# Optimization experiments

Hardware: AMD Instinct MI355X
Metric: run time of the kernel (lower is better)

The kernel has to match this reference:

```python
import jax, jax.numpy as jnp
import numpy as np

N = 4096      # batch size (PK-sampled)
D = 1024      # feature dim
K = 4         # instances per identity
NUM_IDS = N // K


def setup_inputs() -> dict:
    key = jax.random.key(0)
    inputs = jax.random.normal(key, (N, D), dtype=jnp.float32)
    # PK-structured labels: NUM_IDS identities, K instances each.
    targets = jnp.repeat(jnp.arange(NUM_IDS, dtype=jnp.int32), K)
    # Flags alternate within each identity -> every (same/diff id) x (same/diff flag)
    # combination is non-empty for every anchor row.
    flags = jnp.tile(jnp.array([0, 1, 0, 1], dtype=jnp.int32), N // 4)
    epoch = 10  # unused by the loss, kept for signature fidelity
    return {"inputs": inputs, "targets": targets, "flags": flags, "epoch": epoch}


def reference(inputs, targets, flags, epoch):
    # Pairwise Euclidean distances: ||a||^2 + ||b||^2 - 2 a.b, clamped + sqrt.
    sq = jnp.sum(inputs * inputs, axis=1, keepdims=True)          # [n,1]
    dist = sq + sq.T - 2.0 * (inputs @ inputs.T)                   # [n,n]
    dist = jnp.sqrt(jnp.clip(dist, 1e-12, None))

    same_id = targets[:, None] == targets[None, :]                 # mask_1
    same_fl = flags[:, None] == flags[None, :]                     # mask_2
    m_same_hp = same_id & same_fl
    m_same_hn = (~same_id) & same_fl
    m_dif_hp = same_id & (~same_fl)
    m_dif_hn = (~same_id) & (~same_fl)

    NEG = jnp.asarray(-jnp.inf, dist.dtype)
    POS = jnp.asarray(jnp.inf, dist.dtype)
    dist_same_ap = jnp.max(jnp.where(m_same_hp, dist, NEG), axis=1)
    dist_same_an = jnp.min(jnp.where(m_same_hn, dist, POS), axis=1)
    dist_dif_ap = jnp.max(jnp.where(m_dif_hp, dist, NEG), axis=1)
    dist_dif_an = jnp.min(jnp.where(m_dif_hn, dist, POS), axis=1)

    # torch: first index in the FULL row equal to the masked min (exact equality)
    same_min_idx = jnp.argmax(dist == dist_same_an[:, None], axis=1)  # [n]
    dif_min_idx = jnp.argmax(dist == dist_dif_an[:, None], axis=1)    # [n]
    dist_dif_neg = dist[same_min_idx, dif_min_idx]                    # [n]

    relu = jax.nn.relu
    # MarginRankingLoss(x1, x2, y=1) = mean(relu(x2 - x1 + margin))
    loss_same = jnp.mean(relu(dist_same_ap - dist_same_an + 0.8))
    loss_dif = jnp.mean(relu(dist_dif_ap - dist_dif_an + 0.5))
    loss_neg = jnp.mean(relu(dist_same_ap - dist_dif_neg + 0.3))
    return loss_same + loss_dif + loss_neg
```

## Files before the change

### kernel.cpp

```cpp
#include <hip/hip_runtime.h>

#define NROWS 4096
#define DIM   1024

using f32x4 = __attribute__((ext_vector_type(4))) float;
using bfrag = __attribute__((ext_vector_type(8))) short;

__device__ __forceinline__ unsigned short f2bf(float f) {
  unsigned u = __float_as_uint(f);
  u += 0x7fffu + ((u >> 16) & 1u);
  return (unsigned short)(u >> 16);
}
__device__ __forceinline__ float bf2f(unsigned short b) {
  return __uint_as_float(((unsigned)b) << 16);
}
__device__ __forceinline__ unsigned long long shflx64(unsigned long long v, int m) {
  int lo = __shfl_xor((int)(unsigned)(v & 0xffffffffull), m);
  int hi = __shfl_xor((int)(unsigned)(v >> 32), m);
  return ((unsigned long long)(unsigned)hi << 32) | (unsigned)lo;
}

__global__ void prep_kernel(const float* __restrict__ X, unsigned short* __restrict__ Xb,
                            float* __restrict__ sqv, int* maxS, int* maxD,
                            unsigned long long* minS, unsigned long long* minD,
                            float* out) {
  int row = blockIdx.x, t = threadIdx.x;
  float4 v = reinterpret_cast<const float4*>(X + (size_t)row * DIM)[t];
  unsigned short b0 = f2bf(v.x), b1 = f2bf(v.y), b2 = f2bf(v.z), b3 = f2bf(v.w);
  float f0 = bf2f(b0), f1 = bf2f(b1), f2 = bf2f(b2), f3 = bf2f(b3);
  float s = f0 * f0 + f1 * f1 + f2 * f2 + f3 * f3;
  reinterpret_cast<ushort4*>(Xb + (size_t)row * DIM)[t] = make_ushort4(b0, b1, b2, b3);
  for (int m = 32; m; m >>= 1) s += __shfl_xor(s, m);
  __shared__ float ws4[4];
  if ((t & 63) == 0) ws4[t >> 6] = s;
  __syncthreads();
  if (t == 0) {
    sqv[row] = (ws4[0] + ws4[1]) + (ws4[2] + ws4[3]);
    maxS[row] = 0; maxD[row] = 0; minS[row] = ~0ull; minD[row] = ~0ull;
    if (row == 0) out[0] = 0.f;
  }
}

__global__ __launch_bounds__(256, 4) void gram_kernel(
    const unsigned short* __restrict__ Xb, const float* __restrict__ sqv,
    const int* __restrict__ tg, const int* __restrict__ fl,
    int* maxS, int* maxD, unsigned long long* minS, unsigned long long* minD) {
  __shared__ __attribute__((aligned(16))) char smem[32768];
  __shared__ float srow[128], scol[128];
  __shared__ int rtagp[128], ctagp[128];

  int tm = 0, g = blockIdx.x, rem = 32;
  while (g >= rem) { g -= rem; rem--; tm++; }
  int tn = tm + g;
  const int row0 = tm * 128, col0 = tn * 128;
  const int tid = threadIdx.x;
  const int wave = tid >> 6, lane = tid & 63;
  const int q = lane >> 4, li = lane & 15;

  if (tid < 128) {
    srow[tid] = sqv[row0 + tid];
    rtagp[tid] = (fl[row0 + tid] << 12) | tg[row0 + tid];
  } else {
    int c = tid - 128;
    scol[c] = sqv[col0 + c];
    ctagp[c] = (fl[col0 + c] << 12) | tg[col0 + c];
  }

  unsigned short (*As)[64] = (unsigned short (*)[64])smem;
  unsigned short (*Bs)[64] = (unsigned short (*)[64])(smem + 16384);
  float* Ds = (float*)smem;

  f32x4 acc[4][4] = {};
  const int wr = (wave >> 1) * 64, wc = (wave & 1) * 64;
  const int ksrc = ((lane & 7) ^ (lane >> 3)) * 8;

  for (int ks = 0; ks < DIM; ks += 64) {
    __syncthreads();
#pragma unroll
    for (int qq = 0; qq < 4; ++qq) {
      int base = (wave * 4 + qq) * 1024;
      int r = (base >> 7) + (lane >> 3);
      const unsigned short* srcA = Xb + (size_t)(row0 + r) * DIM + ks + ksrc;
      __builtin_amdgcn_global_load_lds(
          (const __attribute__((address_space(1))) void*)srcA,
          (__attribute__((address_space(3))) void*)(smem + base), 16, 0, 0);
      const unsigned short* srcB = Xb + (size_t)(col0 + r) * DIM + ks + ksrc;
      __builtin_amdgcn_global_load_lds(
          (const __attribute__((address_space(1))) void*)srcB,
          (__attribute__((address_space(3))) void*)(smem + 16384 + base), 16, 0, 0);
    }
    __syncthreads();
#pragma unroll
    for (int kk = 0; kk < 2; ++kk) {
      bfrag a[4], b[4];
      int kel = ((kk * 4 + q) ^ (lane & 7)) * 8;
#pragma unroll
      for (int m = 0; m < 4; ++m)
        a[m] = *(const bfrag*)&As[wr + m * 16 + li][kel];
#pragma unroll
      for (int n = 0; n < 4; ++n)
        b[n] = *(const bfrag*)&Bs[wc + n * 16 + li][kel];
#pragma unroll
      for (int m = 0; m < 4; ++m)
#pragma unroll
        for (int n = 0; n < 4; ++n)
          acc[m][n] = __builtin_amdgcn_mfma_f32_16x16x32_bf16(a[m], b[n], acc[m][n], 0, 0, 0);
    }
  }
  __syncthreads();

  float cmxS[4], cmxD[4];
  unsigned long long cmnS[4], cmnD[4];
#pragma unroll
  for (int n = 0; n < 4; ++n) { cmxS[n] = -1.f; cmxD[n] = -1.f; cmnS[n] = ~0ull; cmnD[n] = ~0ull; }
  int ctv[4]; float scv[4];
#pragma unroll
  for (int n = 0; n < 4; ++n) { int lc = wc + n * 16 + li; ctv[n] = ctagp[lc]; scv[n] = scol[lc]; }

#pragma unroll
  for (int h = 0; h < 2; ++h) {
    if ((wave >> 1) == h) {
#pragma unroll
      for (int m = 0; m < 4; ++m)
#pragma unroll
        for (int r = 0; r < 4; ++r) {
          int lr = wr + m * 16 + q * 4 + r;
          int rl = lr & 63;
          int rt = rtagp[lr];
          float sr = srow[lr];
          unsigned long long rbase = (unsigned)(row0 + lr);
#pragma unroll
          for (int n = 0; n < 4; ++n) {
            float d = sqrtf(fmaxf(sr + scv[n] - 2.0f * acc[m][n][r], 1e-12f));
            Ds[rl * 128 + ((wc + n * 16 + li) ^ (lr & 31))] = d;
            int x = rt ^ ctv[n];
            unsigned long long pk = ((unsigned long long)__float_as_uint(d) << 32) | rbase;
            if ((x & 0xFFF) == 0) {
              if ((x >> 12) == 0) cmxS[n] = fmaxf(cmxS[n], d);
              else                cmxD[n] = fmaxf(cmxD[n], d);
            } else {
              if ((x >> 12) == 0) { if (pk < cmnS[n]) cmnS[n] = pk; }
              else                { if (pk < cmnD[n]) cmnD[n] = pk; }
            }
          }
        }
    }
    __syncthreads();
    {
      int rl = (wave & 1) * 32 + (lane & 31);
      int j = (wave >> 1) * 2 + (lane >> 5);
      int rt = rtagp[h * 64 + rl];
      float mxS = -1.f, mxD = -1.f;
      unsigned long long mnS = ~0ull, mnD = ~0ull;
      for (int i = 0; i < 32; ++i) {
        int c = j * 32 + i;
        float d = Ds[rl * 128 + (c ^ (rl & 31))];
        int x = rt ^ ctagp[c];
        unsigned long long pk =
            ((unsigned long long)__float_as_uint(d) << 32) | (unsigned)(col0 + c);
        if ((x & 0xFFF) == 0) { if ((x >> 12) == 0) mxS = fmaxf(mxS, d); else mxD = fmaxf(mxD, d); }
        else { if ((x >> 12) == 0) { if (pk < mnS) mnS = pk; } else { if (pk < mnD) mnD = pk; } }
      }
      mxS = fmaxf(mxS, __shfl_xor(mxS, 32));
      mxD = fmaxf(mxD, __shfl_xor(mxD, 32));
      unsigned long long o = shflx64(mnS, 32); if (o < mnS) mnS = o;
      o = shflx64(mnD, 32); if (o < mnD) mnD = o;
      if (lane < 32) {
        int gr = row0 + h * 64 + rl;
        atomicMax(&maxS[gr], __float_as_int(mxS));
        atomicMax(&maxD[gr], __float_as_int(mxD));
        atomicMin(&minS[gr], mnS);
        atomicMin(&minD[gr], mnD);
      }
    }
    __syncthreads();
  }

#pragma unroll
  for (int n = 0; n < 4; ++n) {
    cmxS[n] = fmaxf(cmxS[n], __shfl_xor(cmxS[n], 16));
    cmxD[n] = fmaxf(cmxD[n], __shfl_xor(cmxD[n], 16));
    unsigned long long o = shflx64(cmnS[n], 16); if (o < cmnS[n]) cmnS[n] = o;
    o = shflx64(cmnD[n], 16); if (o < cmnD[n]) cmnD[n] = o;
    cmxS[n] = fmaxf(cmxS[n], __shfl_xor(cmxS[n], 32));
    cmxD[n] = fmaxf(cmxD[n], __shfl_xor(cmxD[n], 32));
    o = shflx64(cmnS[n], 32); if (o < cmnS[n]) cmnS[n] = o;
    o = shflx64(cmnD[n], 32); if (o < cmnD[n]) cmnD[n] = o;
    if (lane < 16) {
      int gc = col0 + wc + n * 16 + lane;
      atomicMax(&maxS[gc], __float_as_int(cmxS[n]));
      atomicMax(&maxD[gc], __float_as_int(cmxD[n]));
      atomicMin(&minS[gc], cmnS[n]);
      atomicMin(&minD[gc], cmnD[n]);
    }
  }
}

__global__ void finish_kernel(const unsigned short* __restrict__ Xb,
                              const float* __restrict__ sqv,
                              const int* __restrict__ maxS, const int* __restrict__ maxD,
                              const unsigned long long* __restrict__ minS,
                              const unsigned long long* __restrict__ minD, float* out) {
  int wave = threadIdx.x >> 6, lane = threadIdx.x & 63;
  float part = 0.f;
  for (int rr = 0; rr < 8; ++rr) {
    int row = blockIdx.x * 32 + wave * 8 + rr;
    unsigned long long pS = minS[row], pD = minD[row];
    int ia = (int)(pS & 0xffffffffull);
    int ib = (int)(pD & 0xffffffffull);
    const ushort4* pa = (const ushort4*)(Xb + (size_t)ia * DIM);
    const ushort4* pb = (const ushort4*)(Xb + (size_t)ib * DIM);
    float s = 0.f;
#pragma unroll
    for (int qq = 0; qq < 4; ++qq) {
      ushort4 a = pa[lane + qq * 64], b = pb[lane + qq * 64];
      s += bf2f(a.x) * bf2f(b.x) + bf2f(a.y) * bf2f(b.y) +
           bf2f(a.z) * bf2f(b.z) + bf2f(a.w) * bf2f(b.w);
    }
    for (int m = 32; m; m >>= 1) s += __shfl_xor(s, m);
    if (lane == 0) {
      float dneg = sqrtf(fmaxf(sqv[ia] + sqv[ib] - 2.f * s, 1e-12f));
      float mS = __int_as_float(maxS[row]);
      float mD = __int_as_float(maxD[row]);
      float mnSv = __uint_as_float((unsigned)(pS >> 32));
      float mnDv = __uint_as_float((unsigned)(pD >> 32));
      part += fmaxf(mS - mnSv + 0.8f, 0.f) + fmaxf(mD - mnDv + 0.5f, 0.f) +
              fmaxf(mS - dneg + 0.3f, 0.f);
    }
  }
  __shared__ float wp[4];
  if (lane == 0) wp[wave] = part;
  __syncthreads();
  if (threadIdx.x == 0)
    atomicAdd(out, ((wp[0] + wp[1]) + (wp[2] + wp[3])) * (1.0f / 4096.0f));
}

extern "C" void kernel_launch(void* const* d_in, const int* in_sizes, int n_in,
                              void* d_out, int out_size, void* d_ws, size_t ws_size,
                              hipStream_t stream) {
  const float* X = (const float*)d_in[0];
  const int* tg  = (const int*)d_in[1];
  const int* fl  = (const int*)d_in[2];
  float* out = (float*)d_out;

  char* w = (char*)d_ws;
  unsigned short* Xb = (unsigned short*)(w);
  float* sqv = (float*)(w + 8388608);
  int* maxS  = (int*)(w + 8404992);
  int* maxD  = (int*)(w + 8421376);
  unsigned long long* minS = (unsigned long long*)(w + 8437760);
  unsigned long long* minD = (unsigned long long*)(w + 8470528);

  prep_kernel<<<NROWS, 256, 0, stream>>>(X, Xb, sqv, maxS, maxD, minS, minD, out);
  gram_kernel<<<528, 256, 0, stream>>>(Xb, sqv, tg, fl, maxS, maxD, minS, minD);
  finish_kernel<<<128, 256, 0, stream>>>(Xb, sqv, maxS, maxD, minS, minD, out);
}
```

Baseline: 165.9 us.

## Double-buffer gram K-loop, remap tile order, and move column reduction into half-loop

Replaces the single-buffered 64-wide K loop with a double-buffered 32-wide pipeline. The next stage's global-to-LDS load is issued before the MFMA body on the current buffer, so each step needs one barrier instead of two. The LDS layout changes to a k-chunk-major arrangement without the XOR swizzle, and triangular tile indices are computed by sqrt with an interleaved block ordering. Per-column reduction state now lives only inside the active half, to cut register pressure, and launch bounds drop to 3 waves per SIMD. Risks include LDS bank conflicts from the unswizzled layout and lower occupancy.

```diff
diff --git a/kernel.cpp b/kernel.cpp
--- a/kernel.cpp
+++ b/kernel.cpp
@@ -41,7 +41,36 @@
   }
 }
 
-__global__ __launch_bounds__(256, 4) void gram_kernel(
+#define STAGE(BASE, KS)                                                         \
+  {                                                                             \
+    _Pragma("unroll")                                                           \
+    for (int qp = 0; qp < 2; ++qp) {                                            \
+      int ldso = (wave * 2 + qp) * 1024;                                        \
+      int rsrc = qp * 64 + lane;                                                \
+      const unsigned short* sA = Xb + (size_t)(row0 + rsrc) * DIM + (KS) + wave * 8; \
+      __builtin_amdgcn_global_load_lds(                                         \
+          (const __attribute__((address_space(1))) void*)sA,                    \
+          (__attribute__((address_space(3))) void*)((BASE) + ldso), 16, 0, 0);  \
+      const unsigned short* sB = Xb + (size_t)(col0 + rsrc) * DIM + (KS) + wave * 8; \
+      __builtin_amdgcn_global_load_lds(                                         \
+          (const __attribute__((address_space(1))) void*)sB,                    \
+          (__attribute__((address_space(3))) void*)((BASE) + 8192 + ldso), 16, 0, 0); \
+    }                                                                           \
+  }
+
+#define BODY(BASE)                                                              \
+  {                                                                             \
+    bfrag a[4], b[4];                                                           \
+    _Pragma("unroll") for (int m = 0; m < 4; ++m)                               \
+      a[m] = *(const bfrag*)((BASE) + q * 2048 + (wr + m * 16 + li) * 16);      \
+    _Pragma("unroll") for (int n = 0; n < 4; ++n)                               \
+      b[n] = *(const bfrag*)((BASE) + 8192 + q * 2048 + (wc + n * 16 + li) * 16); \
+    _Pragma("unroll") for (int m = 0; m < 4; ++m)                               \
+      _Pragma("unroll") for (int n = 0; n < 4; ++n)                             \
+        acc[m][n] = __builtin_amdgcn_mfma_f32_16x16x32_bf16(a[m], b[n], acc[m][n], 0, 0, 0); \
+  }
+
+__global__ __launch_bounds__(256, 3) void gram_kernel(
     const unsigned short* __restrict__ Xb, const float* __restrict__ sqv,
     const int* __restrict__ tg, const int* __restrict__ fl,
     int* maxS, int* maxD, unsigned long long* minS, unsigned long long* minD) {
@@ -49,9 +78,11 @@
   __shared__ float srow[128], scol[128];
   __shared__ int rtagp[128], ctagp[128];
 
-  int tm = 0, g = blockIdx.x, rem = 32;
-  while (g >= rem) { g -= rem; rem--; tm++; }
-  int tn = tm + g;
+  int g = (blockIdx.x & 7) * 66 + (blockIdx.x >> 3);
+  int tn = (int)((sqrtf(8.f * g + 1.f) - 1.f) * 0.5f);
+  while ((tn + 1) * (tn + 2) / 2 <= g) ++tn;
+  while (tn * (tn + 1) / 2 > g) --tn;
+  int tm = g - tn * (tn + 1) / 2;
   const int row0 = tm * 128, col0 = tn * 128;
   const int tid = threadIdx.x;
   const int wave = tid >> 6, lane = tid & 63;
@@ -66,60 +97,36 @@
     ctagp[c] = (fl[col0 + c] << 12) | tg[col0 + c];
   }
 
-  unsigned short (*As)[64] = (unsigned short (*)[64])smem;
-  unsigned short (*Bs)[64] = (unsigned short (*)[64])(smem + 16384);
+  char* B0 = smem;
+  char* B1 = smem + 16384;
   float* Ds = (float*)smem;
 
   f32x4 acc[4][4] = {};
   const int wr = (wave >> 1) * 64, wc = (wave & 1) * 64;
-  const int ksrc = ((lane & 7) ^ (lane >> 3)) * 8;
-
-  for (int ks = 0; ks < DIM; ks += 64) {
-    __syncthreads();
-#pragma unroll
-    for (int qq = 0; qq < 4; ++qq) {
-      int base = (wave * 4 + qq) * 1024;
-      int r = (base >> 7) + (lane >> 3);
-      const unsigned short* srcA = Xb + (size_t)(row0 + r) * DIM + ks + ksrc;
-      __builtin_amdgcn_global_load_lds(
-          (const __attribute__((address_space(1))) void*)srcA,
-          (__attribute__((address_space(3))) void*)(smem + base), 16, 0, 0);
-      const unsigned short* srcB = Xb + (size_t)(col0 + r) * DIM + ks + ksrc;
-      __builtin_amdgcn_global_load_lds(
-          (const __attribute__((address_space(1))) void*)srcB,
-          (__attribute__((address_space(3))) void*)(smem + 16384 + base), 16, 0, 0);
-    }
-    __syncthreads();
-#pragma unroll
-    for (int kk = 0; kk < 2; ++kk) {
-      bfrag a[4], b[4];
-      int kel = ((kk * 4 + q) ^ (lane & 7)) * 8;
-#pragma unroll
-      for (int m = 0; m < 4; ++m)
-        a[m] = *(const bfrag*)&As[wr + m * 16 + li][kel];
-#pragma unroll
-      for (int n = 0; n < 4; ++n)
-        b[n] = *(const bfrag*)&Bs[wc + n * 16 + li][kel];
-#pragma unroll
-      for (int m = 0; m < 4; ++m)
-#pragma unroll
-        for (int n = 0; n < 4; ++n)
-          acc[m][n] = __builtin_amdgcn_mfma_f32_16x16x32_bf16(a[m], b[n], acc[m][n], 0, 0, 0);
-    }
-  }
+
+  STAGE(B0, 0);
   __syncthreads();
-
-  float cmxS[4], cmxD[4];
-  unsigned long long cmnS[4], cmnD[4];
-#pragma unroll
-  for (int n = 0; n < 4; ++n) { cmxS[n] = -1.f; cmxD[n] = -1.f; cmnS[n] = ~0ull; cmnD[n] = ~0ull; }
-  int ctv[4]; float scv[4];
-#pragma unroll
-  for (int n = 0; n < 4; ++n) { int lc = wc + n * 16 + li; ctv[n] = ctagp[lc]; scv[n] = scol[lc]; }
+  for (int tt = 0; tt < 16; ++tt) {
+    int s0 = tt * 2;
+    STAGE(B1, (s0 + 1) * 32);
+    BODY(B0);
+    __syncthreads();
+    if (tt < 15) STAGE(B0, (s0 + 2) * 32);
+    BODY(B1);
+    __syncthreads();
+  }
 
 #pragma unroll
   for (int h = 0; h < 2; ++h) {
     if ((wave >> 1) == h) {
+      float cmxS[4], cmxD[4];
+      unsigned long long cmnS[4], cmnD[4];
+      int ctv[4]; float scv[4];
+#pragma unroll
+      for (int n = 0; n < 4; ++n) {
+        cmxS[n] = -1.f; cmxD[n] = -1.f; cmnS[n] = ~0ull; cmnD[n] = ~0ull;
+        int lc = wc + n * 16 + li; ctv[n] = ctagp[lc]; scv[n] = scol[lc];
+      }
 #pragma unroll
       for (int m = 0; m < 4; ++m)
 #pragma unroll
@@ -132,7 +139,7 @@
 #pragma unroll
           for (int n = 0; n < 4; ++n) {
             float d = sqrtf(fmaxf(sr + scv[n] - 2.0f * acc[m][n][r], 1e-12f));
-            Ds[rl * 128 + ((wc + n * 16 + li) ^ (lr & 31))] = d;
+            Ds[rl * 128 + ((wc + n * 16 + li) ^ (rl & 31))] = d;
             int x = rt ^ ctv[n];
             unsigned long long pk = ((unsigned long long)__float_as_uint(d) << 32) | rbase;
             if ((x & 0xFFF) == 0) {
@@ -144,6 +151,24 @@
             }
           }
         }
+#pragma unroll
+      for (int n = 0; n < 4; ++n) {
+        cmxS[n] = fmaxf(cmxS[n], __shfl_xor(cmxS[n], 16));
+        cmxD[n] = fmaxf(cmxD[n], __shfl_xor(cmxD[n], 16));
+        unsigned long long o = shflx64(cmnS[n], 16); if (o < cmnS[n]) cmnS[n] = o;
+        o = shflx64(cmnD[n], 16); if (o < cmnD[n]) cmnD[n] = o;
+        cmxS[n] = fmaxf(cmxS[n], __shfl_xor(cmxS[n], 32));
+        cmxD[n] = fmaxf(cmxD[n], __shfl_xor(cmxD[n], 32));
+        o = shflx64(cmnS[n], 32); if (o < cmnS[n]) cmnS[n] = o;
+        o = shflx64(cmnD[n], 32); if (o < cmnD[n]) cmnD[n] = o;
+        if (lane < 16) {
+          int gc = col0 + wc + n * 16 + lane;
+          atomicMax(&maxS[gc], __float_as_int(cmxS[n]));
+          atomicMax(&maxD[gc], __float_as_int(cmxD[n]));
+          atomicMin(&minS[gc], cmnS[n]);
+          atomicMin(&minD[gc], cmnD[n]);
+        }
+      }
     }
     __syncthreads();
     {
@@ -174,25 +199,6 @@
       }
     }
     __syncthreads();
-  }
-
-#pragma unroll
-  for (int n = 0; n < 4; ++n) {
-    cmxS[n] = fmaxf(cmxS[n], __shfl_xor(cmxS[n], 16));
-    cmxD[n] = fmaxf(cmxD[n], __shfl_xor(cmxD[n], 16));
-    unsigned long long o = shflx64(cmnS[n], 16); if (o < cmnS[n]) cmnS[n] = o;
-    o = shflx64(cmnD[n], 16); if (o < cmnD[n]) cmnD[n] = o;
-    cmxS[n] = fmaxf(cmxS[n], __shfl_xor(cmxS[n], 32));
-    cmxD[n] = fmaxf(cmxD[n], __shfl_xor(cmxD[n], 32));
-    o = shflx64(cmnS[n], 32); if (o < cmnS[n]) cmnS[n] = o;
-    o = shflx64(cmnD[n], 32); if (o < cmnD[n]) cmnD[n] = o;
-    if (lane < 16) {
-      int gc = col0 + wc + n * 16 + lane;
-      atomicMax(&maxS[gc], __float_as_int(cmxS[n]));
-      atomicMax(&maxD[gc], __float_as_int(cmxD[n]));
-      atomicMin(&minS[gc], cmnS[n]);
-      atomicMin(&minD[gc], cmnD[n]);
-    }
   }
 }
 
```

New measurement: 188.4 us. 13.6% more time.

## Replace LDS-staged row reduction in gram epilogue with register shuffles

Applied to the files above, without the earlier changes.

The epilogue no longer writes the distance tile to shared memory and re-reads it for the per-row max/min. Each lane now keeps per-row partial reductions in registers, combines them across the 16 column lanes with xor shuffles, and issues row atomics from lane li==0. This drops the two-phase LDS pass and its barriers, at the cost of more shuffles and more row atomics (one per wave per row instead of one per row per half-tile). The launch-bounds occupancy hint of 4 is also removed, and the staging loop is moved into a macro.

```diff
diff --git a/kernel.cpp b/kernel.cpp
--- a/kernel.cpp
+++ b/kernel.cpp
@@ -41,7 +41,24 @@
   }
 }
 
-__global__ __launch_bounds__(256, 4) void gram_kernel(
+#define STAGE(KS)                                                                \
+  {                                                                              \
+    _Pragma("unroll")                                                            \
+    for (int qq = 0; qq < 4; ++qq) {                                             \
+      int boff = (wave * 4 + qq) * 1024;                     \
+      int r = (wave * 4 + qq) * 8 + (lane >> 3);        \
+      const unsigned short* sA = Xb + (size_t)(row0 + r) * DIM + (KS) + ksrc;    \
+      __builtin_amdgcn_global_load_lds(                                          \
+          (const __attribute__((address_space(1))) void*)sA,                     \
+          (__attribute__((address_space(3))) void*)(smem + boff), 16, 0, 0);     \
+      const unsigned short* sB = Xb + (size_t)(col0 + r) * DIM + (KS) + ksrc;    \
+      __builtin_amdgcn_global_load_lds(                                          \
+          (const __attribute__((address_space(1))) void*)sB,                     \
+          (__attribute__((address_space(3))) void*)(smem + 16384 + boff), 16, 0, 0); \
+    }                                                                            \
+  }
+
+__global__ __launch_bounds__(256) void gram_kernel(
     const unsigned short* __restrict__ Xb, const float* __restrict__ sqv,
     const int* __restrict__ tg, const int* __restrict__ fl,
     int* maxS, int* maxD, unsigned long long* minS, unsigned long long* minD) {
@@ -56,6 +73,7 @@
   const int tid = threadIdx.x;
   const int wave = tid >> 6, lane = tid & 63;
   const int q = lane >> 4, li = lane & 15;
+  const int ksrc = ((lane & 7) ^ (lane >> 3)) * 8;
 
   if (tid < 128) {
     srow[tid] = sqv[row0 + tid];
@@ -68,27 +86,13 @@
 
   unsigned short (*As)[64] = (unsigned short (*)[64])smem;
   unsigned short (*Bs)[64] = (unsigned short (*)[64])(smem + 16384);
-  float* Ds = (float*)smem;
 
   f32x4 acc[4][4] = {};
   const int wr = (wave >> 1) * 64, wc = (wave & 1) * 64;
-  const int ksrc = ((lane & 7) ^ (lane >> 3)) * 8;
 
   for (int ks = 0; ks < DIM; ks += 64) {
     __syncthreads();
-#pragma unroll
-    for (int qq = 0; qq < 4; ++qq) {
-      int base = (wave * 4 + qq) * 1024;
-      int r = (base >> 7) + (lane >> 3);
-      const unsigned short* srcA = Xb + (size_t)(row0 + r) * DIM + ks + ksrc;
-      __builtin_amdgcn_global_load_lds(
-          (const __attribute__((address_space(1))) void*)srcA,
-          (__attribute__((address_space(3))) void*)(smem + base), 16, 0, 0);
-      const unsigned short* srcB = Xb + (size_t)(col0 + r) * DIM + ks + ksrc;
-      __builtin_amdgcn_global_load_lds(
-          (const __attribute__((address_space(1))) void*)srcB,
-          (__attribute__((address_space(3))) void*)(smem + 16384 + base), 16, 0, 0);
-    }
+    STAGE(ks);
     __syncthreads();
 #pragma unroll
     for (int kk = 0; kk < 2; ++kk) {
@@ -107,85 +111,64 @@
           acc[m][n] = __builtin_amdgcn_mfma_f32_16x16x32_bf16(a[m], b[n], acc[m][n], 0, 0, 0);
     }
   }
-  __syncthreads();
 
   float cmxS[4], cmxD[4];
   unsigned long long cmnS[4], cmnD[4];
-#pragma unroll
-  for (int n = 0; n < 4; ++n) { cmxS[n] = -1.f; cmxD[n] = -1.f; cmnS[n] = ~0ull; cmnD[n] = ~0ull; }
   int ctv[4]; float scv[4];
 #pragma unroll
-  for (int n = 0; n < 4; ++n) { int lc = wc + n * 16 + li; ctv[n] = ctagp[lc]; scv[n] = scol[lc]; }
-
-#pragma unroll
-  for (int h = 0; h < 2; ++h) {
-    if ((wave >> 1) == h) {
-#pragma unroll
-      for (int m = 0; m < 4; ++m)
-#pragma unroll
-        for (int r = 0; r < 4; ++r) {
-          int lr = wr + m * 16 + q * 4 + r;
-          int rl = lr & 63;
-          int rt = rtagp[lr];
-          float sr = srow[lr];
-          unsigned long long rbase = (unsigned)(row0 + lr);
-#pragma unroll
-          for (int n = 0; n < 4; ++n) {
-            float d = sqrtf(fmaxf(sr + scv[n] - 2.0f * acc[m][n][r], 1e-12f));
-            Ds[rl * 128 + ((wc + n * 16 + li) ^ (lr & 31))] = d;
-            int x = rt ^ ctv[n];
-            unsigned long long pk = ((unsigned long long)__float_as_uint(d) << 32) | rbase;
-            if ((x & 0xFFF) == 0) {
-              if ((x >> 12) == 0) cmxS[n] = fmaxf(cmxS[n], d);
-              else                cmxD[n] = fmaxf(cmxD[n], d);
-            } else {
-              if ((x >> 12) == 0) { if (pk < cmnS[n]) cmnS[n] = pk; }
-              else                { if (pk < cmnD[n]) cmnD[n] = pk; }
-            }
-          }
+  for (int n = 0; n < 4; ++n) {
+    cmxS[n] = -1.f; cmxD[n] = -1.f; cmnS[n] = ~0ull; cmnD[n] = ~0ull;
+    int lc = wc + n * 16 + li; ctv[n] = ctagp[lc]; scv[n] = scol[lc];
+  }
+#pragma unroll
+  for (int m = 0; m < 4; ++m)
+#pragma unroll
+    for (int r = 0; r < 4; ++r) {
+      int lr = wr + m * 16 + q * 4 + r;
+      int rt = rtagp[lr];
+      float sr = srow[lr];
+      unsigned long long rbase = (unsigned)(row0 + lr);
+      float rmxS = -1.f, rmxD = -1.f;
+      unsigned long long rmnS = ~0ull, rmnD = ~0ull;
+#pragma unroll
+      for (int n = 0; n < 4; ++n) {
+        float d = sqrtf(fmaxf(sr + scv[n] - 2.0f * acc[m][n][r], 1e-12f));
+        int x = rt ^ ctv[n];
+        unsigned long long db = (unsigned long long)__float_as_uint(d) << 32;
+        unsigned long long pkr = db | (unsigned)(col0 + wc + n * 16 + li);
+        unsigned long long pkc = db | rbase;
+        if ((x & 0xFFF) == 0) {
+          if ((x >> 12) == 0) { rmxS = fmaxf(rmxS, d); cmxS[n] = fmaxf(cmxS[n], d); }
+          else                { rmxD = fmaxf(rmxD, d); cmxD[n] = fmaxf(cmxD[n], d); }
+        } else {
+          if ((x >> 12) == 0) { if (pkr < rmnS) rmnS = pkr; if (pkc < cmnS[n]) cmnS[n] = pkc; }
+          else                { if (pkr < rmnD) rmnD = pkr; if (pkc < cmnD[n]) cmnD[n] = pkc; }
         }
-    }
-    __syncthreads();
-    {
-      int rl = (wave & 1) * 32 + (lane & 31);
-      int j = (wave >> 1) * 2 + (lane >> 5);
-      int rt = rtagp[h * 64 + rl];
-      float mxS = -1.f, mxD = -1.f;
-      unsigned long long mnS = ~0ull, mnD = ~0ull;
-      for (int i = 0; i < 32; ++i) {
-        int c = j * 32 + i;
-        float d = Ds[rl * 128 + (c ^ (rl & 31))];
-        int x = rt ^ ctagp[c];
-        unsigned long long pk =
-            ((unsigned long long)__float_as_uint(d) << 32) | (unsigned)(col0 + c);
-        if ((x & 0xFFF) == 0) { if ((x >> 12) == 0) mxS = fmaxf(mxS, d); else mxD = fmaxf(mxD, d); }
-        else { if ((x >> 12) == 0) { if (pk < mnS) mnS = pk; } else { if (pk < mnD) mnD = pk; } }
       }
-      mxS = fmaxf(mxS, __shfl_xor(mxS, 32));
-      mxD = fmaxf(mxD, __shfl_xor(mxD, 32));
-      unsigned long long o = shflx64(mnS, 32); if (o < mnS) mnS = o;
-      o = shflx64(mnD, 32); if (o < mnD) mnD = o;
-      if (lane < 32) {
-        int gr = row0 + h * 64 + rl;
-        atomicMax(&maxS[gr], __float_as_int(mxS));
-        atomicMax(&maxD[gr], __float_as_int(mxD));
-        atomicMin(&minS[gr], mnS);
-        atomicMin(&minD[gr], mnD);
+#pragma unroll
+      for (int mk = 1; mk <= 8; mk <<= 1) {
+        rmxS = fmaxf(rmxS, __shfl_xor(rmxS, mk));
+        rmxD = fmaxf(rmxD, __shfl_xor(rmxD, mk));
+        unsigned long long o = shflx64(rmnS, mk); if (o < rmnS) rmnS = o;
+        o = shflx64(rmnD, mk); if (o < rmnD) rmnD = o;
       }
-    }
-    __syncthreads();
-  }
-
+      if (li == 0) {
+        int gr = row0 + lr;
+        atomicMax(&maxS[gr], __float_as_int(rmxS));
+        atomicMax(&maxD[gr], __float_as_int(rmxD));
+        atomicMin(&minS[gr], rmnS);
+        atomicMin(&minD[gr], rmnD);
+      }
+    }
 #pragma unroll
   for (int n = 0; n < 4; ++n) {
-    cmxS[n] = fmaxf(cmxS[n], __shfl_xor(cmxS[n], 16));
-    cmxD[n] = fmaxf(cmxD[n], __shfl_xor(cmxD[n], 16));
-    unsigned long long o = shflx64(cmnS[n], 16); if (o < cmnS[n]) cmnS[n] = o;
-    o = shflx64(cmnD[n], 16); if (o < cmnD[n]) cmnD[n] = o;
-    cmxS[n] = fmaxf(cmxS[n], __shfl_xor(cmxS[n], 32));
-    cmxD[n] = fmaxf(cmxD[n], __shfl_xor(cmxD[n], 32));
-    o = shflx64(cmnS[n], 32); if (o < cmnS[n]) cmnS[n] = o;
-    o = shflx64(cmnD[n], 32); if (o < cmnD[n]) cmnD[n] = o;
+#pragma unroll
+    for (int mk = 16; mk <= 32; mk <<= 1) {
+      cmxS[n] = fmaxf(cmxS[n], __shfl_xor(cmxS[n], mk));
+      cmxD[n] = fmaxf(cmxD[n], __shfl_xor(cmxD[n], mk));
+      unsigned long long o = shflx64(cmnS[n], mk); if (o < cmnS[n]) cmnS[n] = o;
+      o = shflx64(cmnD[n], mk); if (o < cmnD[n]) cmnD[n] = o;
+    }
     if (lane < 16) {
       int gc = col0 + wc + n * 16 + lane;
       atomicMax(&maxS[gc], __float_as_int(cmxS[n]));
```

Result: faster. 149.5 us (-9.9%).
